# Optimization experiments

Measured on AMD Instinct MI355X. Metric: run time of the kernel, lower is better.

The kernel has to match this reference:

```python
import jax, jax.numpy as jnp
import numpy as np

B, S, D, H = 4, 2048, 1024, 16
DH = D // H
LN_EPS = 1e-5


def setup_inputs() -> dict:
    key = jax.random.key(0)
    ks = jax.random.split(key, 8)
    q = jax.random.normal(ks[0], (B, S, D), dtype=jnp.float32)
    k = jax.random.normal(ks[1], (B, S, D), dtype=jnp.float32)
    v = jax.random.normal(ks[2], (B, S, D), dtype=jnp.float32)
    masks = jax.random.randint(ks[3], (B, S, S), 0, 2, dtype=jnp.int32)
    proj_Q = jax.random.normal(ks[4], (D,), dtype=jnp.float32)
    proj_K = jax.random.normal(ks[5], (D,), dtype=jnp.float32)
    proj_V = jax.random.normal(ks[6], (D,), dtype=jnp.float32)
    gamma = jnp.ones((D,), dtype=jnp.float32)
    beta = jnp.zeros((D,), dtype=jnp.float32)
    return {"q": q, "k": k, "v": v, "masks": masks,
            "proj_Q": proj_Q, "proj_K": proj_K, "proj_V": proj_V,
            "gamma": gamma, "beta": beta}


def _split_heads(x):
    # x: [B,S,D] -> permute(0,2,1) -> [B,D,S] -> view(B*H, DH, S) -> permute -> [B*H, S, DH]
    xt = jnp.transpose(x, (0, 2, 1))              # [B,D,S]
    xt = xt.reshape(B * H, DH, S)                 # [B*H,DH,S] (batch-major head split)
    return jnp.transpose(xt, (0, 2, 1))           # [B*H,S,DH]


def reference(q, k, v, masks, proj_Q, proj_K, proj_V, gamma, beta):
    # Source bug preserved: projections all applied to `x` == q; k, v are ignored.
    x = q
    Qh = _split_heads(x * proj_Q)                 # [B*H,S,DH]
    Kh = _split_heads(x * proj_K)
    Vh = _split_heads(x * proj_V)

    # masks cat'd along dim 0 num_head times (head-major tiling, as in source)
    m = jnp.tile(masks, (H, 1, 1)).astype(bool)   # [H*B,S,S]

    scores = jnp.einsum('nqd,nkd->nqk', Qh, Kh) / jnp.sqrt(jnp.float32(D))
    scores = jnp.where(m, jnp.float32(-1e-10), scores)  # source uses -1e-10, not -inf
    attn = jax.nn.softmax(scores, axis=2)
    ctx = jnp.einsum('nqk,nkd->nqd', attn, Vh)    # [B*H,S,DH]

    # merge heads back: [B*H,S,DH] -> [B*H,DH,S] -> [B,D,S] -> [B,S,D]
    ctx = jnp.transpose(ctx, (0, 2, 1)).reshape(B, D, S)
    ctx = jnp.transpose(ctx, (0, 2, 1))

    out = ctx + q                                  # dropout(p=0) is identity
    mu = jnp.mean(out, axis=-1, keepdims=True)
    var = jnp.var(out, axis=-1, keepdims=True)
    out = (out - mu) * jax.lax.rsqrt(var + LN_EPS) * gamma + beta
    return out
```

## Files before the change

### kernel.cpp

```cpp
#include <hip/hip_runtime.h>
#include <math.h>

#define Bn 4
#define Sn 2048
#define Dn 1024
#define Hn 16
#define DHn 64
#define QT 128
#define KT 64
#define STR 72

typedef __attribute__((ext_vector_type(8))) short short8;
typedef __attribute__((ext_vector_type(4))) float f32x4;

__device__ __forceinline__ ushort f2bf(float f) {
    union { float f; unsigned u; } x; x.f = f;
    unsigned r = x.u + 0x7fffu + ((x.u >> 16) & 1u);
    return (ushort)(r >> 16);
}

__device__ __forceinline__ unsigned pack_bf2(float lo, float hi) {
    unsigned r;
    asm("v_cvt_pk_bf16_f32 %0, %1, %2" : "=v"(r) : "v"(lo), "v"(hi));
    return r;
}

__device__ __forceinline__ float fexp2(float x) { return __builtin_amdgcn_exp2f(x); }

__device__ __forceinline__ float mask_sel(unsigned nib, int r, float s) {
    int sx; unsigned tb;
    asm("v_bfe_i32 %0, %1, %2, 1" : "=v"(sx) : "v"(nib), "i"(r));
    asm("v_bfi_b32 %0, %1, 0, %2" : "=v"(tb) : "v"(sx), "v"(__float_as_uint(s)));
    return __uint_as_float(tb);
}

__global__ __launch_bounds__(256)
void prep_fused(const float* __restrict__ xin, const float* __restrict__ pK,
                const float* __restrict__ pV, const int* __restrict__ masks,
                ushort* __restrict__ Kw, ushort* __restrict__ Vw,
                unsigned long long* __restrict__ mpack)
{
    __shared__ ushort LK[64 * STR];
    __shared__ ushort LV[64 * STR];
    const int t = threadIdx.x;

    if (blockIdx.x >= 2048) {
        const int l = t & 63;
        const int wid_g = ((blockIdx.x - 2048) * 256 + t) >> 6;
        #pragma unroll 4
        for (int i = 0; i < 16; ++i) {
            int word = wid_g * 16 + i;
            int row  = word >> 5, wd = word & 31;
            int m = masks[(size_t)row * 2048 + wd * 64 + l];
            unsigned long long bits = __ballot(m != 0);
            if (l == 0) mpack[word] = bits;
        }
        return;
    }

    const int kt = blockIdx.x & 31, n = blockIdx.x >> 5, b = n >> 4, h = n & 15;
    const int sl = t >> 2, dq = (t & 3) * 16;

    const float* xp  = xin + ((size_t)b * Sn + kt * 64 + sl) * Dn + h * DHn + dq;
    const float* pkp = pK + h * DHn + dq;
    const float* pvp = pV + h * DHn + dq;

    float xv[16], pk[16], pv[16];
    #pragma unroll
    for (int j = 0; j < 4; ++j) {
        float4 a  = ((const float4*)xp)[j];
        float4 kk = ((const float4*)pkp)[j];
        float4 vv = ((const float4*)pvp)[j];
        xv[4*j+0] = a.x;  xv[4*j+1] = a.y;  xv[4*j+2] = a.z;  xv[4*j+3] = a.w;
        pk[4*j+0] = kk.x; pk[4*j+1] = kk.y; pk[4*j+2] = kk.z; pk[4*j+3] = kk.w;
        pv[4*j+0] = vv.x; pv[4*j+1] = vv.y; pv[4*j+2] = vv.z; pv[4*j+3] = vv.w;
    }
    unsigned kw[8], vw[8];
    #pragma unroll
    for (int j = 0; j < 8; ++j) {
        kw[j] = pack_bf2(xv[2*j] * pk[2*j], xv[2*j+1] * pk[2*j+1]);
        vw[j] = pack_bf2(xv[2*j] * pv[2*j], xv[2*j+1] * pv[2*j+1]);
    }
    *(uint4*)&LK[sl * STR + dq]     = make_uint4(kw[0], kw[1], kw[2], kw[3]);
    *(uint4*)&LK[sl * STR + dq + 8] = make_uint4(kw[4], kw[5], kw[6], kw[7]);
    *(uint4*)&LV[sl * STR + dq]     = make_uint4(vw[0], vw[1], vw[2], vw[3]);
    *(uint4*)&LV[sl * STR + dq + 8] = make_uint4(vw[4], vw[5], vw[6], vw[7]);
    __syncthreads();

    ushort* kout = Kw + ((size_t)n * 32 + kt) * 4096;
    ushort* vout = Vw + ((size_t)n * 32 + kt) * 4096;
    #pragma unroll
    for (int i = 0; i < 2; ++i) {
        int c  = t * 2 + i;
        int f  = c >> 6, lc = c & 63;
        int key = (f >> 1) * 16 + (lc & 15);
        int dh0 = (f & 1) * 32 + (lc >> 4) * 8;
        *(uint4*)(kout + c * 8) = *(const uint4*)&LK[key * STR + dh0];
        int dg = f & 3, hh = f >> 2;
        int dhv = dg * 16 + (lc & 15);
        ushort tmp[8];
        #pragma unroll
        for (int e = 0; e < 8; ++e) {
            int p  = hh * 32 + (lc >> 4) * 8 + e;
            int ss = (p & 32) | ((p & 4) << 2) | ((p & 24) >> 1) | (p & 3);
            tmp[e] = LV[ss * STR + dhv];
        }
        unsigned o0 = (unsigned)tmp[0] | ((unsigned)tmp[1] << 16);
        unsigned o1 = (unsigned)tmp[2] | ((unsigned)tmp[3] << 16);
        unsigned o2 = (unsigned)tmp[4] | ((unsigned)tmp[5] << 16);
        unsigned o3 = (unsigned)tmp[6] | ((unsigned)tmp[7] << 16);
        *(uint4*)(vout + c * 8) = make_uint4(o0, o1, o2, o3);
    }
}

__global__ __launch_bounds__(256, 3)
void attn_fast3(const float* __restrict__ xin, const unsigned long long* __restrict__ mpack,
                const float* __restrict__ pQ, const ushort* __restrict__ Kw,
                const ushort* __restrict__ Vw, float* __restrict__ out)
{
    __shared__ __attribute__((aligned(16))) ushort S[16384];

    const int id   = blockIdx.x;
    const int xcd  = id & 7, pos = id >> 3;
    const int n    = (pos >> 4) * 8 + xcd;
    const int q0   = (pos & 15) * 128;
    const int b    = n >> 4;
    const int h    = n & 15;
    const int mb   = n & 3;

    const int t  = threadIdx.x;
    const int w  = t >> 6;
    const int l  = t & 63;
    const int G  = l >> 4;
    const int li = l & 15;
    const int G4 = G * 4;
    const int G4p16 = G4 + 16;

    const float C2 = 0.0450842200277800f;
    const float* xb = xin + (size_t)b * Sn * Dn + h * DHn;
    const float pq_s = pQ[h * DHn + l] * C2;
    #pragma unroll
    for (int i = 0; i < 8; ++i) {
        #pragma unroll
        for (int j = 0; j < 4; ++j) {
            int qr = i * 4 + j;
            float v = xb[(size_t)(q0 + w * 32 + qr) * Dn + l];
            S[(w * 32 + qr) * STR + l] = f2bf(v * pq_s);
        }
    }
    short8 qf[2][2];
    #pragma unroll
    for (int qs = 0; qs < 2; ++qs)
        #pragma unroll
        for (int kk = 0; kk < 2; ++kk)
            qf[qs][kk] = *(const short8*)&S[(w*32 + qs*16 + li) * STR + kk*32 + G*8];
    __syncthreads();

    const f32x4 Z4 = {0.f, 0.f, 0.f, 0.f};
    const short8 VONES = {(short)0x3F80, (short)0x3F80, (short)0x3F80, (short)0x3F80,
                          (short)0x3F80, (short)0x3F80, (short)0x3F80, (short)0x3F80};

    f32x4 acc_o[2][4];
    f32x4 acc_l[2];
    #pragma unroll
    for (int qs = 0; qs < 2; ++qs) {
        #pragma unroll
        for (int dg = 0; dg < 4; ++dg) acc_o[qs][dg] = (f32x4){0.f, 0.f, 0.f, 0.f};
        acc_l[qs] = (f32x4){0.f, 0.f, 0.f, 0.f};
    }

    const ushort* kwf = Kw + (size_t)n * 131072 + (w * 2) * 512 + (size_t)l * 8;
    const ushort* vwf = Vw + (size_t)n * 131072 + (w * 2) * 512 + (size_t)l * 8;
    const int fo0 = (w * 2) * 512 + l * 8;
    const int fo1 = (w * 2 + 1) * 512 + l * 8;

    const int row0 = q0 + w * 32 + li;
    const unsigned long long* mrow0 = mpack + (size_t)(mb * 2048 + row0) * 32;
    const unsigned long long* mrow1 = mpack + (size_t)(mb * 2048 + row0 + 16) * 32;

    unsigned long long mA0, mA1, mB0, mB1;

    {
        short8 a = *(const short8*)kwf;
        short8 c = *(const short8*)(kwf + 512);
        short8 d = *(const short8*)vwf;
        short8 e = *(const short8*)(vwf + 512);
        mA0 = mrow0[0]; mA1 = mrow1[0];
        *(short8*)&S[fo0] = a;
        *(short8*)&S[fo1] = c;
        *(short8*)&S[8192 + fo0] = d;
        *(short8*)&S[8192 + fo1] = e;
    }

#define BODY(CUR, NXT, MC0, MC1, MN0, MN1, KTv, PF)                                   \
    {                                                                                  \
        __syncthreads();                     \
               \
        f32x4 s_[2][4];                                                                \
        __builtin_amdgcn_s_setprio(1);                                                 \
        _Pragma("unroll")                                                              \
        for (int kg = 0; kg < 4; ++kg) {                                               \
            short8 kf0 = *(const short8*)&S[(CUR)*4096 + (kg*2+0)*512 + l*8];          \
            short8 kf1 = *(const short8*)&S[(CUR)*4096 + (kg*2+1)*512 + l*8];          \
            s_[0][kg] = __builtin_amdgcn_mfma_f32_16x16x32_bf16(kf0, qf[0][0], Z4, 0, 0, 0); \
            s_[1][kg] = __builtin_amdgcn_mfma_f32_16x16x32_bf16(kf0, qf[1][0], Z4, 0, 0, 0); \
            s_[0][kg] = __builtin_amdgcn_mfma_f32_16x16x32_bf16(kf1, qf[0][1], s_[0][kg], 0, 0, 0); \
            s_[1][kg] = __builtin_amdgcn_mfma_f32_16x16x32_bf16(kf1, qf[1][1], s_[1][kg], 0, 0, 0); \
        }                                                                              \
        __builtin_amdgcn_s_setprio(0);                                                 \
                        \
        short8 kst0, kst1, vst0, vst1;                                                 \
        if (PF) {                                                                      \
            const ushort* kp = kwf + (size_t)((KTv)+1) * 4096;                         \
            const ushort* vp = vwf + (size_t)((KTv)+1) * 4096;                         \
            kst0 = *(const short8*)kp;  kst1 = *(const short8*)(kp + 512);             \
            vst0 = *(const short8*)vp;  vst1 = *(const short8*)(vp + 512);             \
            MN0 = mrow0[(KTv)+1];       MN1 = mrow1[(KTv)+1];                          \
        }                                                                              \
                       \
        short8 pf[2][2];                                                               \
        _Pragma("unroll")                                                              \
        for (int qs = 0; qs < 2; ++qs) {                                               \
            unsigned mlo = (unsigned)(qs ? (MC1) : (MC0));                             \
            unsigned mhi = (unsigned)((qs ? (MC1) : (MC0)) >> 32);                     \
            float ev[16];                                                              \
            _Pragma("unroll")                                                          \
            for (int kg = 0; kg < 4; ++kg) {                                           \
                unsigned dwh = (kg < 2) ? mlo : mhi;                                   \
                unsigned nib;                                                          \
                asm("v_bfe_u32 %0, %1, %2, 4" : "=v"(nib)                              \
                    : "v"(dwh), "v"((kg & 1) ? G4p16 : G4));                           \
                _Pragma("unroll")                                                      \
                for (int r = 0; r < 4; ++r)                                            \
                    ev[kg*4 + r] = fexp2(mask_sel(nib, r, s_[qs][kg][r]));             \
            }                                                                          \
            _Pragma("unroll")                                                          \
            for (int hh = 0; hh < 2; ++hh) {                                           \
                union { unsigned u[4]; short8 v; } pu;                                 \
                pu.u[0] = pack_bf2(ev[hh*8+0], ev[hh*8+1]);                            \
                pu.u[1] = pack_bf2(ev[hh*8+2], ev[hh*8+3]);                            \
                pu.u[2] = pack_bf2(ev[hh*8+4], ev[hh*8+5]);                            \
                pu.u[3] = pack_bf2(ev[hh*8+6], ev[hh*8+7]);                            \
                pf[qs][hh] = pu.v;                                                     \
            }                                                                          \
        }                                                                              \
                                                \
        __builtin_amdgcn_s_setprio(1);                                                 \
        _Pragma("unroll")                                                              \
        for (int hh = 0; hh < 2; ++hh) {                                               \
            short8 vf0 = *(const short8*)&S[8192 + (CUR)*4096 + (hh*4+0)*512 + l*8];   \
            short8 vf1 = *(const short8*)&S[8192 + (CUR)*4096 + (hh*4+1)*512 + l*8];   \
            short8 vf2 = *(const short8*)&S[8192 + (CUR)*4096 + (hh*4+2)*512 + l*8];   \
            short8 vf3 = *(const short8*)&S[8192 + (CUR)*4096 + (hh*4+3)*512 + l*8];   \
            _Pragma("unroll")                                                          \
            for (int qs = 0; qs < 2; ++qs) {                                           \
                acc_o[qs][0] = __builtin_amdgcn_mfma_f32_16x16x32_bf16(pf[qs][hh], vf0, acc_o[qs][0], 0, 0, 0); \
                acc_o[qs][1] = __builtin_amdgcn_mfma_f32_16x16x32_bf16(pf[qs][hh], vf1, acc_o[qs][1], 0, 0, 0); \
                acc_o[qs][2] = __builtin_amdgcn_mfma_f32_16x16x32_bf16(pf[qs][hh], vf2, acc_o[qs][2], 0, 0, 0); \
                acc_o[qs][3] = __builtin_amdgcn_mfma_f32_16x16x32_bf16(pf[qs][hh], vf3, acc_o[qs][3], 0, 0, 0); \
                acc_l[qs]    = __builtin_amdgcn_mfma_f32_16x16x32_bf16(pf[qs][hh], VONES, acc_l[qs], 0, 0, 0); \
            }                                                                          \
        }                                                                              \
        __builtin_amdgcn_s_setprio(0);                                                 \
                                     \
        if (PF) {                                                                      \
            *(short8*)&S[(NXT)*4096 + fo0] = kst0;                                     \
            *(short8*)&S[(NXT)*4096 + fo1] = kst1;                                     \
            *(short8*)&S[8192 + (NXT)*4096 + fo0] = vst0;                              \
            *(short8*)&S[8192 + (NXT)*4096 + fo1] = vst1;                              \
        }                                                                              \
    }

    for (int kt = 0; kt < 32; kt += 2) {
        BODY(0, 1, mA0, mA1, mB0, mB1, kt, true)
        BODY(1, 0, mB0, mB1, mA0, mA1, kt + 1, (kt + 1 < 31))
    }
#undef BODY

    #pragma unroll
    for (int qs = 0; qs < 2; ++qs) {
        #pragma unroll
        for (int r = 0; r < 4; ++r) {
            float inv = 1.f / acc_l[qs][r];
            int qg = q0 + w*32 + qs*16 + G4 + r;
            float* ob = out + ((size_t)b * Sn + qg) * Dn + h * DHn;
            #pragma unroll
            for (int dg = 0; dg < 4; ++dg)
                ob[dg*16 + li] = acc_o[qs][dg][r] * inv;
        }
    }
}

__global__ __launch_bounds__(256)
void prep_kv(const float* __restrict__ xin, const float* __restrict__ pK,
             const float* __restrict__ pV, ushort* __restrict__ Kbf,
             ushort* __restrict__ Vtw)
{
    __shared__ ushort Ls[64 * STR];
    const int n = blockIdx.y, b = n >> 4, h = n & 15;
    const int s0 = blockIdx.x * 64;
    const int t = threadIdx.x;
    const int sl = t >> 2, dq = (t & 3) * 16;

    const float* xp = xin + (size_t)b * Sn * Dn + (size_t)(s0 + sl) * Dn + h * DHn + dq;
    const float* pkp = pK + h * DHn + dq;
    const float* pvp = pV + h * DHn + dq;

    float xv[16], pk[16], pv[16];
    #pragma unroll
    for (int j = 0; j < 4; ++j) {
        float4 a = ((const float4*)xp)[j];
        float4 kk = ((const float4*)pkp)[j];
        float4 vv = ((const float4*)pvp)[j];
        xv[4*j+0] = a.x;  xv[4*j+1] = a.y;  xv[4*j+2] = a.z;  xv[4*j+3] = a.w;
        pk[4*j+0] = kk.x; pk[4*j+1] = kk.y; pk[4*j+2] = kk.z; pk[4*j+3] = kk.w;
        pv[4*j+0] = vv.x; pv[4*j+1] = vv.y; pv[4*j+2] = vv.z; pv[4*j+3] = vv.w;
    }
    unsigned kw[8], vw[8];
    #pragma unroll
    for (int j = 0; j < 8; ++j) {
        kw[j] = pack_bf2(xv[2*j] * pk[2*j], xv[2*j+1] * pk[2*j+1]);
        vw[j] = pack_bf2(xv[2*j] * pv[2*j], xv[2*j+1] * pv[2*j+1]);
    }
    ushort* kdst = Kbf + ((size_t)n * Sn + s0 + sl) * DHn + dq;
    *(uint4*)kdst       = make_uint4(kw[0], kw[1], kw[2], kw[3]);
    *(uint4*)(kdst + 8) = make_uint4(kw[4], kw[5], kw[6], kw[7]);

    *(uint4*)&Ls[sl * STR + dq]     = make_uint4(vw[0], vw[1], vw[2], vw[3]);
    *(uint4*)&Ls[sl * STR + dq + 8] = make_uint4(vw[4], vw[5], vw[6], vw[7]);
    __syncthreads();

    const int dh = t >> 2, p4 = t & 3;
    ushort ov[16];
    #pragma unroll
    for (int j = 0; j < 16; ++j) {
        int p  = p4 * 16 + j;
        int ss = (p & 32) | ((p & 4) << 2) | ((p & 24) >> 1) | (p & 3);
        ov[j] = Ls[ss * STR + dh];
    }
    unsigned ow[8];
    #pragma unroll
    for (int j = 0; j < 8; ++j) ow[j] = (unsigned)ov[2*j] | ((unsigned)ov[2*j+1] << 16);
    ushort* vdst = Vtw + ((size_t)n * DHn + dh) * Sn + s0 + p4 * 16;
    *(uint4*)vdst       = make_uint4(ow[0], ow[1], ow[2], ow[3]);
    *(uint4*)(vdst + 8) = make_uint4(ow[4], ow[5], ow[6], ow[7]);
}

__global__ __launch_bounds__(256, 4)
void attn_fast2(const float* __restrict__ xin, const int* __restrict__ masks,
                const float* __restrict__ pQ, const ushort* __restrict__ Kbf,
                const ushort* __restrict__ Vtw, float* __restrict__ out)
{
    __shared__ ushort Ks[KT * STR];
    __shared__ ushort Vts[DHn * STR];

    const int n  = blockIdx.y;
    const int b  = n >> 4;
    const int h  = n & 15;
    const int mb = n & 3;
    const int q0 = blockIdx.x * QT;

    const int t  = threadIdx.x;
    const int w  = t >> 6;
    const int l  = t & 63;
    const int G  = l >> 4;
    const int li = l & 15;

    const float C2 = 0.0450842200277800f;
    const float* xb = xin + (size_t)b * Sn * Dn + h * DHn;
    const float pq_s = pQ[h * DHn + l] * C2;
    ushort* qstage = ((w < 2) ? Ks : Vts) + (w & 1) * (32 * STR);
    #pragma unroll
    for (int i = 0; i < 8; ++i) {
        #pragma unroll
        for (int j = 0; j < 4; ++j) {
            int qr = i * 4 + j;
            float v = xb[(size_t)(q0 + w * 32 + qr) * Dn + l];
            qstage[qr * STR + l] = f2bf(v * pq_s);
        }
    }
    short8 qf[2][2];
    #pragma unroll
    for (int qs = 0; qs < 2; ++qs)
        #pragma unroll
        for (int kk = 0; kk < 2; ++kk)
            qf[qs][kk] = *(const short8*)&qstage[(qs*16 + li) * STR + kk*32 + G*8];

    f32x4 acc_o[2][4];
    float lsum[2];
    #pragma unroll
    for (int qs = 0; qs < 2; ++qs) {
        #pragma unroll
        for (int dg = 0; dg < 4; ++dg) acc_o[qs][dg] = (f32x4){0.f, 0.f, 0.f, 0.f};
        lsum[qs] = 0.f;
    }

    const int* mq = masks + (size_t)mb * Sn * Sn + (size_t)(q0 + w*32 + li) * Sn;

    const int srow = w * 16 + (l >> 2);
    const int part = (l & 3) * 16;
    const ushort* ksrc = Kbf + (size_t)n * Sn * DHn + (size_t)srow * DHn + part;
    const ushort* vsrc = Vtw + (size_t)n * DHn * Sn + (size_t)srow * Sn + part;
    ushort* kdst = &Ks[srow * STR + part];
    ushort* vdst = &Vts[srow * STR + part];

    for (int kt = 0; kt < Sn / KT; ++kt) {
        __syncthreads();
        const ushort* kp = ksrc + (size_t)kt * KT * DHn;
        const ushort* vp = vsrc + kt * KT;
        short8 k0 = *(const short8*)kp, k1 = *(const short8*)(kp + 8);
        short8 v0 = *(const short8*)vp, v1 = *(const short8*)(vp + 8);
        *(short8*)kdst       = k0;
        *(short8*)(kdst + 8) = k1;
        *(short8*)vdst       = v0;
        *(short8*)(vdst + 8) = v1;
        __syncthreads();

        f32x4 s[2][4];
        #pragma unroll
        for (int qs = 0; qs < 2; ++qs)
            #pragma unroll
            for (int kg = 0; kg < 4; ++kg) s[qs][kg] = (f32x4){0.f, 0.f, 0.f, 0.f};
        __builtin_amdgcn_s_setprio(1);
        #pragma unroll
        for (int kg = 0; kg < 4; ++kg) {
            #pragma unroll
            for (int kk = 0; kk < 2; ++kk) {
                short8 kf = *(const short8*)&Ks[(kg*16 + li) * STR + kk*32 + G*8];
                s[0][kg] = __builtin_amdgcn_mfma_f32_16x16x32_bf16(kf, qf[0][kk], s[0][kg], 0, 0, 0);
                s[1][kg] = __builtin_amdgcn_mfma_f32_16x16x32_bf16(kf, qf[1][kk], s[1][kg], 0, 0, 0);
            }
        }
        __builtin_amdgcn_s_setprio(0);

        short8 pf[2][2];
        #pragma unroll
        for (int qs = 0; qs < 2; ++qs) {
            int4 mv[4];
            #pragma unroll
            for (int kg = 0; kg < 4; ++kg)
                mv[kg] = *(const int4*)(mq + (size_t)qs*16*Sn + kt*KT + kg*16 + G*4);
            float ev[16];
            #pragma unroll
            for (int kg = 0; kg < 4; ++kg) {
                int ma[4] = {mv[kg].x, mv[kg].y, mv[kg].z, mv[kg].w};
                #pragma unroll
                for (int r = 0; r < 4; ++r) {
                    float tt = ma[r] ? 0.f : s[qs][kg][r];
                    ev[kg*4 + r] = fexp2(tt);
                }
            }
            lsum[qs] += (((ev[0]+ev[1])+(ev[2]+ev[3])) + ((ev[4]+ev[5])+(ev[6]+ev[7])))
                      + (((ev[8]+ev[9])+(ev[10]+ev[11])) + ((ev[12]+ev[13])+(ev[14]+ev[15])));
            #pragma unroll
            for (int hh = 0; hh < 2; ++hh) {
                union { unsigned u[4]; short8 v; } pu;
                pu.u[0] = pack_bf2(ev[hh*8+0], ev[hh*8+1]);
                pu.u[1] = pack_bf2(ev[hh*8+2], ev[hh*8+3]);
                pu.u[2] = pack_bf2(ev[hh*8+4], ev[hh*8+5]);
                pu.u[3] = pack_bf2(ev[hh*8+6], ev[hh*8+7]);
                pf[qs][hh] = pu.v;
            }
        }

        #pragma unroll
        for (int hh = 0; hh < 2; ++hh) {
            short8 vf[4];
            #pragma unroll
            for (int dg = 0; dg < 4; ++dg)
                vf[dg] = *(const short8*)&Vts[(dg*16 + li) * STR + hh*32 + G*8];
            __builtin_amdgcn_s_setprio(1);
            #pragma unroll
            for (int qs = 0; qs < 2; ++qs)
                #pragma unroll
                for (int dg = 0; dg < 4; ++dg)
                    acc_o[qs][dg] = __builtin_amdgcn_mfma_f32_16x16x32_bf16(pf[qs][hh], vf[dg], acc_o[qs][dg], 0, 0, 0);
            __builtin_amdgcn_s_setprio(0);
        }
    }

    #pragma unroll
    for (int qs = 0; qs < 2; ++qs) {
        float v = lsum[qs];
        v += __shfl_xor(v, 16, 64);
        v += __shfl_xor(v, 32, 64);
        lsum[qs] = v;
    }

    #pragma unroll
    for (int qs = 0; qs < 2; ++qs) {
        #pragma unroll
        for (int r = 0; r < 4; ++r) {
            float lv = __shfl(lsum[qs], (l & 48) | (G * 4 + r), 64);
            float inv = 1.f / lv;
            int qg = q0 + w*32 + qs*16 + G*4 + r;
            float* ob = out + ((size_t)b * Sn + qg) * Dn + h * DHn;
            #pragma unroll
            for (int dg = 0; dg < 4; ++dg)
                ob[dg*16 + li] = acc_o[qs][dg][r] * inv;
        }
    }
}

__global__ __launch_bounds__(256)
void ln_kernel(const float* __restrict__ qin, const float* __restrict__ gamma,
               const float* __restrict__ beta, float* __restrict__ out)
{
    const int row = blockIdx.x;
    const int t   = threadIdx.x;
    const size_t base = (size_t)row * Dn + t * 4;

    float4 c = *(const float4*)(out + base);
    float4 r = *(const float4*)(qin + base);
    float4 v = make_float4(c.x + r.x, c.y + r.y, c.z + r.z, c.w + r.w);

    float sum = v.x + v.y + v.z + v.w;
    float sq  = v.x * v.x + v.y * v.y + v.z * v.z + v.w * v.w;
    #pragma unroll
    for (int off = 32; off >= 1; off >>= 1) {
        sum += __shfl_xor(sum, off, 64);
        sq  += __shfl_xor(sq,  off, 64);
    }
    __shared__ float as_[4], aq_[4];
    const int wid = t >> 6, ln = t & 63;
    if (ln == 0) { as_[wid] = sum; aq_[wid] = sq; }
    __syncthreads();
    sum = as_[0] + as_[1] + as_[2] + as_[3];
    sq  = aq_[0] + aq_[1] + aq_[2] + aq_[3];

    const float mean = sum * (1.f / Dn);
    const float var  = sq * (1.f / Dn) - mean * mean;
    const float rstd = rsqrtf(var + 1e-5f);

    float4 ga = *(const float4*)(gamma + t * 4);
    float4 be = *(const float4*)(beta + t * 4);
    float4 o;
    o.x = (v.x - mean) * rstd * ga.x + be.x;
    o.y = (v.y - mean) * rstd * ga.y + be.y;
    o.z = (v.z - mean) * rstd * ga.z + be.z;
    o.w = (v.w - mean) * rstd * ga.w + be.w;
    *(float4*)(out + base) = o;
}

extern "C" void kernel_launch(void* const* d_in, const int* in_sizes, int n_in,
                              void* d_out, int out_size, void* d_ws, size_t ws_size,
                              hipStream_t stream) {
    const float* q     = (const float*)d_in[0];
    const int*   masks = (const int*)d_in[3];
    const float* pQ    = (const float*)d_in[4];
    const float* pK    = (const float*)d_in[5];
    const float* pV    = (const float*)d_in[6];
    const float* gamma = (const float*)d_in[7];
    const float* beta  = (const float*)d_in[8];
    float* out = (float*)d_out;
    (void)in_sizes; (void)n_in; (void)out_size;

    const size_t elems = (size_t)Bn * Hn * Sn * DHn;
    const size_t kvbytes = elems * 2 * sizeof(ushort);
    const size_t need3 = kvbytes + (size_t)4 * Sn * 32 * 8;

    if (ws_size >= need3) {
        ushort* Kw = (ushort*)d_ws;
        ushort* Vw = Kw + elems;
        unsigned long long* mpack = (unsigned long long*)((char*)d_ws + kvbytes);
        prep_fused<<<6144, 256, 0, stream>>>(q, pK, pV, masks, Kw, Vw, mpack);
        attn_fast3<<<1024, 256, 0, stream>>>(q, mpack, pQ, Kw, Vw, out);
    } else if (ws_size >= kvbytes) {
        ushort* Kbf = (ushort*)d_ws;
        ushort* Vtw = Kbf + elems;
        prep_kv<<<dim3(Sn / 64, Bn * Hn), 256, 0, stream>>>(q, pK, pV, Kbf, Vtw);
        attn_fast2<<<dim3(Sn / QT, Bn * Hn), 256, 0, stream>>>(q, masks, pQ, Kbf, Vtw, out);
    }
    ln_kernel<<<Bn * Sn, 256, 0, stream>>>(q, gamma, beta, out);
}
```

Before: 137.9 us.

## Load K/V fragments directly from global memory instead of staging through LDS

New measurement: 146.8 us. 1.06x slower.

```diff
diff --git a/kernel.cpp b/kernel.cpp
--- a/kernel.cpp
+++ b/kernel.cpp
@@ -114,11 +114,11 @@
 }
 
 __global__ __launch_bounds__(256, 3)
-void attn_fast3(const float* __restrict__ xin, const unsigned long long* __restrict__ mpack,
+void attn_fast4(const float* __restrict__ xin, const unsigned long long* __restrict__ mpack,
                 const float* __restrict__ pQ, const ushort* __restrict__ Kw,
                 const ushort* __restrict__ Vw, float* __restrict__ out)
 {
-    __shared__ __attribute__((aligned(16))) ushort S[16384];
+    __shared__ __attribute__((aligned(16))) ushort S[QT * STR];
 
     const int id   = blockIdx.x;
     const int xcd  = id & 7, pos = id >> 3;
@@ -154,7 +154,6 @@
         #pragma unroll
         for (int kk = 0; kk < 2; ++kk)
             qf[qs][kk] = *(const short8*)&S[(w*32 + qs*16 + li) * STR + kk*32 + G*8];
-    __syncthreads();
 
     const f32x4 Z4 = {0.f, 0.f, 0.f, 0.f};
     const short8 VONES = {(short)0x3F80, (short)0x3F80, (short)0x3F80, (short)0x3F80,
@@ -169,113 +168,78 @@
         acc_l[qs] = (f32x4){0.f, 0.f, 0.f, 0.f};
     }
 
-    const ushort* kwf = Kw + (size_t)n * 131072 + (w * 2) * 512 + (size_t)l * 8;
-    const ushort* vwf = Vw + (size_t)n * 131072 + (w * 2) * 512 + (size_t)l * 8;
-    const int fo0 = (w * 2) * 512 + l * 8;
-    const int fo1 = (w * 2 + 1) * 512 + l * 8;
+    const ushort* kwb = Kw + (size_t)n * 131072 + (size_t)l * 8;
+    const ushort* vwb = Vw + (size_t)n * 131072 + (size_t)l * 8;
 
     const int row0 = q0 + w * 32 + li;
     const unsigned long long* mrow0 = mpack + (size_t)(mb * 2048 + row0) * 32;
     const unsigned long long* mrow1 = mpack + (size_t)(mb * 2048 + row0 + 16) * 32;
 
-    unsigned long long mA0, mA1, mB0, mB1;
-
-    {
-        short8 a = *(const short8*)kwf;
-        short8 c = *(const short8*)(kwf + 512);
-        short8 d = *(const short8*)vwf;
-        short8 e = *(const short8*)(vwf + 512);
-        mA0 = mrow0[0]; mA1 = mrow1[0];
-        *(short8*)&S[fo0] = a;
-        *(short8*)&S[fo1] = c;
-        *(short8*)&S[8192 + fo0] = d;
-        *(short8*)&S[8192 + fo1] = e;
-    }
-
-#define BODY(CUR, NXT, MC0, MC1, MN0, MN1, KTv, PF)                                   \
-    {                                                                                  \
-        __syncthreads();                     \
-               \
-        f32x4 s_[2][4];                                                                \
-        __builtin_amdgcn_s_setprio(1);                                                 \
-        _Pragma("unroll")                                                              \
-        for (int kg = 0; kg < 4; ++kg) {                                               \
-            short8 kf0 = *(const short8*)&S[(CUR)*4096 + (kg*2+0)*512 + l*8];          \
-            short8 kf1 = *(const short8*)&S[(CUR)*4096 + (kg*2+1)*512 + l*8];          \
-            s_[0][kg] = __builtin_amdgcn_mfma_f32_16x16x32_bf16(kf0, qf[0][0], Z4, 0, 0, 0); \
-            s_[1][kg] = __builtin_amdgcn_mfma_f32_16x16x32_bf16(kf0, qf[1][0], Z4, 0, 0, 0); \
-            s_[0][kg] = __builtin_amdgcn_mfma_f32_16x16x32_bf16(kf1, qf[0][1], s_[0][kg], 0, 0, 0); \
-            s_[1][kg] = __builtin_amdgcn_mfma_f32_16x16x32_bf16(kf1, qf[1][1], s_[1][kg], 0, 0, 0); \
-        }                                                                              \
-        __builtin_amdgcn_s_setprio(0);                                                 \
-                        \
-        short8 kst0, kst1, vst0, vst1;                                                 \
-        if (PF) {                                                                      \
-            const ushort* kp = kwf + (size_t)((KTv)+1) * 4096;                         \
-            const ushort* vp = vwf + (size_t)((KTv)+1) * 4096;                         \
-            kst0 = *(const short8*)kp;  kst1 = *(const short8*)(kp + 512);             \
-            vst0 = *(const short8*)vp;  vst1 = *(const short8*)(vp + 512);             \
-            MN0 = mrow0[(KTv)+1];       MN1 = mrow1[(KTv)+1];                          \
-        }                                                                              \
-                       \
-        short8 pf[2][2];                                                               \
-        _Pragma("unroll")                                                              \
-        for (int qs = 0; qs < 2; ++qs) {                                               \
-            unsigned mlo = (unsigned)(qs ? (MC1) : (MC0));                             \
-            unsigned mhi = (unsigned)((qs ? (MC1) : (MC0)) >> 32);                     \
-            float ev[16];                                                              \
-            _Pragma("unroll")                                                          \
-            for (int kg = 0; kg < 4; ++kg) {                                           \
-                unsigned dwh = (kg < 2) ? mlo : mhi;                                   \
-                unsigned nib;                                                          \
-                asm("v_bfe_u32 %0, %1, %2, 4" : "=v"(nib)                              \
-                    : "v"(dwh), "v"((kg & 1) ? G4p16 : G4));                           \
-                _Pragma("unroll")                                                      \
-                for (int r = 0; r < 4; ++r)                                            \
-                    ev[kg*4 + r] = fexp2(mask_sel(nib, r, s_[qs][kg][r]));             \
-            }                                                                          \
-            _Pragma("unroll")                                                          \
-            for (int hh = 0; hh < 2; ++hh) {                                           \
-                union { unsigned u[4]; short8 v; } pu;                                 \
-                pu.u[0] = pack_bf2(ev[hh*8+0], ev[hh*8+1]);                            \
-                pu.u[1] = pack_bf2(ev[hh*8+2], ev[hh*8+3]);                            \
-                pu.u[2] = pack_bf2(ev[hh*8+4], ev[hh*8+5]);                            \
-                pu.u[3] = pack_bf2(ev[hh*8+6], ev[hh*8+7]);                            \
-                pf[qs][hh] = pu.v;                                                     \
-            }                                                                          \
-        }                                                                              \
-                                                \
-        __builtin_amdgcn_s_setprio(1);                                                 \
-        _Pragma("unroll")                                                              \
-        for (int hh = 0; hh < 2; ++hh) {                                               \
-            short8 vf0 = *(const short8*)&S[8192 + (CUR)*4096 + (hh*4+0)*512 + l*8];   \
-            short8 vf1 = *(const short8*)&S[8192 + (CUR)*4096 + (hh*4+1)*512 + l*8];   \
-            short8 vf2 = *(const short8*)&S[8192 + (CUR)*4096 + (hh*4+2)*512 + l*8];   \
-            short8 vf3 = *(const short8*)&S[8192 + (CUR)*4096 + (hh*4+3)*512 + l*8];   \
-            _Pragma("unroll")                                                          \
-            for (int qs = 0; qs < 2; ++qs) {                                           \
-                acc_o[qs][0] = __builtin_amdgcn_mfma_f32_16x16x32_bf16(pf[qs][hh], vf0, acc_o[qs][0], 0, 0, 0); \
-                acc_o[qs][1] = __builtin_amdgcn_mfma_f32_16x16x32_bf16(pf[qs][hh], vf1, acc_o[qs][1], 0, 0, 0); \
-                acc_o[qs][2] = __builtin_amdgcn_mfma_f32_16x16x32_bf16(pf[qs][hh], vf2, acc_o[qs][2], 0, 0, 0); \
-                acc_o[qs][3] = __builtin_amdgcn_mfma_f32_16x16x32_bf16(pf[qs][hh], vf3, acc_o[qs][3], 0, 0, 0); \
-                acc_l[qs]    = __builtin_amdgcn_mfma_f32_16x16x32_bf16(pf[qs][hh], VONES, acc_l[qs], 0, 0, 0); \
-            }                                                                          \
-        }                                                                              \
-        __builtin_amdgcn_s_setprio(0);                                                 \
-                                     \
-        if (PF) {                                                                      \
-            *(short8*)&S[(NXT)*4096 + fo0] = kst0;                                     \
-            *(short8*)&S[(NXT)*4096 + fo1] = kst1;                                     \
-            *(short8*)&S[8192 + (NXT)*4096 + fo0] = vst0;                              \
-            *(short8*)&S[8192 + (NXT)*4096 + fo1] = vst1;                              \
-        }                                                                              \
-    }
-
-    for (int kt = 0; kt < 32; kt += 2) {
-        BODY(0, 1, mA0, mA1, mB0, mB1, kt, true)
-        BODY(1, 0, mB0, mB1, mA0, mA1, kt + 1, (kt + 1 < 31))
-    }
-#undef BODY
+    #pragma unroll 2
+    for (int kt = 0; kt < 32; ++kt) {
+        const ushort* kp = kwb + kt * 4096;
+        const ushort* vp = vwb + kt * 4096;
+        unsigned long long mc0 = mrow0[kt];
+        unsigned long long mc1 = mrow1[kt];
+
+        f32x4 s_[2][4];
+        __builtin_amdgcn_s_setprio(1);
+        #pragma unroll
+        for (int kg = 0; kg < 4; ++kg) {
+            short8 kf0 = *(const short8*)(kp + (kg*2+0)*512);
+            short8 kf1 = *(const short8*)(kp + (kg*2+1)*512);
+            s_[0][kg] = __builtin_amdgcn_mfma_f32_16x16x32_bf16(kf0, qf[0][0], Z4, 0, 0, 0);
+            s_[1][kg] = __builtin_amdgcn_mfma_f32_16x16x32_bf16(kf0, qf[1][0], Z4, 0, 0, 0);
+            s_[0][kg] = __builtin_amdgcn_mfma_f32_16x16x32_bf16(kf1, qf[0][1], s_[0][kg], 0, 0, 0);
+            s_[1][kg] = __builtin_amdgcn_mfma_f32_16x16x32_bf16(kf1, qf[1][1], s_[1][kg], 0, 0, 0);
+        }
+        __builtin_amdgcn_s_setprio(0);
+
+        short8 pf[2][2];
+        #pragma unroll
+        for (int qs = 0; qs < 2; ++qs) {
+            unsigned mlo = (unsigned)(qs ? mc1 : mc0);
+            unsigned mhi = (unsigned)((qs ? mc1 : mc0) >> 32);
+            float ev[16];
+            #pragma unroll
+            for (int kg = 0; kg < 4; ++kg) {
+                unsigned dwh = (kg < 2) ? mlo : mhi;
+                unsigned nib;
+                asm("v_bfe_u32 %0, %1, %2, 4" : "=v"(nib)
+                    : "v"(dwh), "v"((kg & 1) ? G4p16 : G4));
+                #pragma unroll
+                for (int r = 0; r < 4; ++r)
+                    ev[kg*4 + r] = fexp2(mask_sel(nib, r, s_[qs][kg][r]));
+            }
+            #pragma unroll
+            for (int hh = 0; hh < 2; ++hh) {
+                union { unsigned u[4]; short8 v; } pu;
+                pu.u[0] = pack_bf2(ev[hh*8+0], ev[hh*8+1]);
+                pu.u[1] = pack_bf2(ev[hh*8+2], ev[hh*8+3]);
+                pu.u[2] = pack_bf2(ev[hh*8+4], ev[hh*8+5]);
+                pu.u[3] = pack_bf2(ev[hh*8+6], ev[hh*8+7]);
+                pf[qs][hh] = pu.v;
+            }
+        }
+
+        __builtin_amdgcn_s_setprio(1);
+        #pragma unroll
+        for (int hh = 0; hh < 2; ++hh) {
+            short8 vf0 = *(const short8*)(vp + (hh*4+0)*512);
+            short8 vf1 = *(const short8*)(vp + (hh*4+1)*512);
+            short8 vf2 = *(const short8*)(vp + (hh*4+2)*512);
+            short8 vf3 = *(const short8*)(vp + (hh*4+3)*512);
+            #pragma unroll
+            for (int qs = 0; qs < 2; ++qs) {
+                acc_o[qs][0] = __builtin_amdgcn_mfma_f32_16x16x32_bf16(pf[qs][hh], vf0, acc_o[qs][0], 0, 0, 0);
+                acc_o[qs][1] = __builtin_amdgcn_mfma_f32_16x16x32_bf16(pf[qs][hh], vf1, acc_o[qs][1], 0, 0, 0);
+                acc_o[qs][2] = __builtin_amdgcn_mfma_f32_16x16x32_bf16(pf[qs][hh], vf2, acc_o[qs][2], 0, 0, 0);
+                acc_o[qs][3] = __builtin_amdgcn_mfma_f32_16x16x32_bf16(pf[qs][hh], vf3, acc_o[qs][3], 0, 0, 0);
+                acc_l[qs]    = __builtin_amdgcn_mfma_f32_16x16x32_bf16(pf[qs][hh], VONES, acc_l[qs], 0, 0, 0);
+            }
+        }
+        __builtin_amdgcn_s_setprio(0);
+    }
 
     #pragma unroll
     for (int qs = 0; qs < 2; ++qs) {
@@ -564,7 +528,7 @@
         ushort* Vw = Kw + elems;
         unsigned long long* mpack = (unsigned long long*)((char*)d_ws + kvbytes);
         prep_fused<<<6144, 256, 0, stream>>>(q, pK, pV, masks, Kw, Vw, mpack);
-        attn_fast3<<<1024, 256, 0, stream>>>(q, mpack, pQ, Kw, Vw, out);
+        attn_fast4<<<1024, 256, 0, stream>>>(q, mpack, pQ, Kw, Vw, out);
     } else if (ws_size >= kvbytes) {
         ushort* Kbf = (ushort*)d_ws;
         ushort* Vtw = Kbf + elems;
```

## Load K/V fragments directly from global into registers, drop LDS staging

Applied to the files above, without the earlier changes.

New measurement: 146.6 us. 6.3% more time.

```diff
diff --git a/kernel.cpp b/kernel.cpp
--- a/kernel.cpp
+++ b/kernel.cpp
@@ -113,12 +113,12 @@
     }
 }
 
-__global__ __launch_bounds__(256, 3)
-void attn_fast3(const float* __restrict__ xin, const unsigned long long* __restrict__ mpack,
+__global__ __launch_bounds__(256, 2)
+void attn_fast5(const float* __restrict__ xin, const unsigned long long* __restrict__ mpack,
                 const float* __restrict__ pQ, const ushort* __restrict__ Kw,
                 const ushort* __restrict__ Vw, float* __restrict__ out)
 {
-    __shared__ __attribute__((aligned(16))) ushort S[16384];
+    __shared__ __attribute__((aligned(16))) ushort S[QT * STR];
 
     const int id   = blockIdx.x;
     const int xcd  = id & 7, pos = id >> 3;
@@ -154,7 +154,6 @@
         #pragma unroll
         for (int kk = 0; kk < 2; ++kk)
             qf[qs][kk] = *(const short8*)&S[(w*32 + qs*16 + li) * STR + kk*32 + G*8];
-    __syncthreads();
 
     const f32x4 Z4 = {0.f, 0.f, 0.f, 0.f};
     const short8 VONES = {(short)0x3F80, (short)0x3F80, (short)0x3F80, (short)0x3F80,
@@ -169,54 +168,46 @@
         acc_l[qs] = (f32x4){0.f, 0.f, 0.f, 0.f};
     }
 
-    const ushort* kwf = Kw + (size_t)n * 131072 + (w * 2) * 512 + (size_t)l * 8;
-    const ushort* vwf = Vw + (size_t)n * 131072 + (w * 2) * 512 + (size_t)l * 8;
-    const int fo0 = (w * 2) * 512 + l * 8;
-    const int fo1 = (w * 2 + 1) * 512 + l * 8;
+    const ushort* kwb = Kw + (size_t)n * 131072 + (size_t)l * 8;
+    const ushort* vwb = Vw + (size_t)n * 131072 + (size_t)l * 8;
 
     const int row0 = q0 + w * 32 + li;
     const unsigned long long* mrow0 = mpack + (size_t)(mb * 2048 + row0) * 32;
     const unsigned long long* mrow1 = mpack + (size_t)(mb * 2048 + row0 + 16) * 32;
 
+    short8 kA[8], vA[8], kB[8], vB[8];
     unsigned long long mA0, mA1, mB0, mB1;
-
-    {
-        short8 a = *(const short8*)kwf;
-        short8 c = *(const short8*)(kwf + 512);
-        short8 d = *(const short8*)vwf;
-        short8 e = *(const short8*)(vwf + 512);
-        mA0 = mrow0[0]; mA1 = mrow1[0];
-        *(short8*)&S[fo0] = a;
-        *(short8*)&S[fo1] = c;
-        *(short8*)&S[8192 + fo0] = d;
-        *(short8*)&S[8192 + fo1] = e;
-    }
-
-#define BODY(CUR, NXT, MC0, MC1, MN0, MN1, KTv, PF)                                   \
+    #pragma unroll
+    for (int f = 0; f < 8; ++f) {
+        kA[f] = *(const short8*)(kwb + f * 512);
+        vA[f] = *(const short8*)(vwb + f * 512);
+    }
+    mA0 = mrow0[0]; mA1 = mrow1[0];
+
+#define BODY(KC, VC, KN, VN, MC0, MC1, MN0, MN1, KTv, PF)                              \
     {                                                                                  \
-        __syncthreads();                     \
+                  \
+        if (PF) {                                                                      \
+            const ushort* kp = kwb + (size_t)((KTv)+1) * 4096;                         \
+            const ushort* vp = vwb + (size_t)((KTv)+1) * 4096;                         \
+            _Pragma("unroll")                                                          \
+            for (int f = 0; f < 8; ++f) {                                              \
+                KN[f] = *(const short8*)(kp + f * 512);                                \
+                VN[f] = *(const short8*)(vp + f * 512);                                \
+            }                                                                          \
+            MN0 = mrow0[(KTv)+1];  MN1 = mrow1[(KTv)+1];                               \
+        }                                                                              \
                \
         f32x4 s_[2][4];                                                                \
         __builtin_amdgcn_s_setprio(1);                                                 \
         _Pragma("unroll")                                                              \
         for (int kg = 0; kg < 4; ++kg) {                                               \
-            short8 kf0 = *(const short8*)&S[(CUR)*4096 + (kg*2+0)*512 + l*8];          \
-            short8 kf1 = *(const short8*)&S[(CUR)*4096 + (kg*2+1)*512 + l*8];          \
-            s_[0][kg] = __builtin_amdgcn_mfma_f32_16x16x32_bf16(kf0, qf[0][0], Z4, 0, 0, 0); \
-            s_[1][kg] = __builtin_amdgcn_mfma_f32_16x16x32_bf16(kf0, qf[1][0], Z4, 0, 0, 0); \
-            s_[0][kg] = __builtin_amdgcn_mfma_f32_16x16x32_bf16(kf1, qf[0][1], s_[0][kg], 0, 0, 0); \
-            s_[1][kg] = __builtin_amdgcn_mfma_f32_16x16x32_bf16(kf1, qf[1][1], s_[1][kg], 0, 0, 0); \
+            s_[0][kg] = __builtin_amdgcn_mfma_f32_16x16x32_bf16(KC[kg*2+0], qf[0][0], Z4, 0, 0, 0); \
+            s_[1][kg] = __builtin_amdgcn_mfma_f32_16x16x32_bf16(KC[kg*2+0], qf[1][0], Z4, 0, 0, 0); \
+            s_[0][kg] = __builtin_amdgcn_mfma_f32_16x16x32_bf16(KC[kg*2+1], qf[0][1], s_[0][kg], 0, 0, 0); \
+            s_[1][kg] = __builtin_amdgcn_mfma_f32_16x16x32_bf16(KC[kg*2+1], qf[1][1], s_[1][kg], 0, 0, 0); \
         }                                                                              \
         __builtin_amdgcn_s_setprio(0);                                                 \
-                        \
-        short8 kst0, kst1, vst0, vst1;                                                 \
-        if (PF) {                                                                      \
-            const ushort* kp = kwf + (size_t)((KTv)+1) * 4096;                         \
-            const ushort* vp = vwf + (size_t)((KTv)+1) * 4096;                         \
-            kst0 = *(const short8*)kp;  kst1 = *(const short8*)(kp + 512);             \
-            vst0 = *(const short8*)vp;  vst1 = *(const short8*)(vp + 512);             \
-            MN0 = mrow0[(KTv)+1];       MN1 = mrow1[(KTv)+1];                          \
-        }                                                                              \
                        \
         short8 pf[2][2];                                                               \
         _Pragma("unroll")                                                              \
@@ -248,32 +239,21 @@
         __builtin_amdgcn_s_setprio(1);                                                 \
         _Pragma("unroll")                                                              \
         for (int hh = 0; hh < 2; ++hh) {                                               \
-            short8 vf0 = *(const short8*)&S[8192 + (CUR)*4096 + (hh*4+0)*512 + l*8];   \
-            short8 vf1 = *(const short8*)&S[8192 + (CUR)*4096 + (hh*4+1)*512 + l*8];   \
-            short8 vf2 = *(const short8*)&S[8192 + (CUR)*4096 + (hh*4+2)*512 + l*8];   \
-            short8 vf3 = *(const short8*)&S[8192 + (CUR)*4096 + (hh*4+3)*512 + l*8];   \
             _Pragma("unroll")                                                          \
             for (int qs = 0; qs < 2; ++qs) {                                           \
-                acc_o[qs][0] = __builtin_amdgcn_mfma_f32_16x16x32_bf16(pf[qs][hh], vf0, acc_o[qs][0], 0, 0, 0); \
-                acc_o[qs][1] = __builtin_amdgcn_mfma_f32_16x16x32_bf16(pf[qs][hh], vf1, acc_o[qs][1], 0, 0, 0); \
-                acc_o[qs][2] = __builtin_amdgcn_mfma_f32_16x16x32_bf16(pf[qs][hh], vf2, acc_o[qs][2], 0, 0, 0); \
-                acc_o[qs][3] = __builtin_amdgcn_mfma_f32_16x16x32_bf16(pf[qs][hh], vf3, acc_o[qs][3], 0, 0, 0); \
+                acc_o[qs][0] = __builtin_amdgcn_mfma_f32_16x16x32_bf16(pf[qs][hh], VC[hh*4+0], acc_o[qs][0], 0, 0, 0); \
+                acc_o[qs][1] = __builtin_amdgcn_mfma_f32_16x16x32_bf16(pf[qs][hh], VC[hh*4+1], acc_o[qs][1], 0, 0, 0); \
+                acc_o[qs][2] = __builtin_amdgcn_mfma_f32_16x16x32_bf16(pf[qs][hh], VC[hh*4+2], acc_o[qs][2], 0, 0, 0); \
+                acc_o[qs][3] = __builtin_amdgcn_mfma_f32_16x16x32_bf16(pf[qs][hh], VC[hh*4+3], acc_o[qs][3], 0, 0, 0); \
                 acc_l[qs]    = __builtin_amdgcn_mfma_f32_16x16x32_bf16(pf[qs][hh], VONES, acc_l[qs], 0, 0, 0); \
             }                                                                          \
         }                                                                              \
         __builtin_amdgcn_s_setprio(0);                                                 \
-                                     \
-        if (PF) {                                                                      \
-            *(short8*)&S[(NXT)*4096 + fo0] = kst0;                                     \
-            *(short8*)&S[(NXT)*4096 + fo1] = kst1;                                     \
-            *(short8*)&S[8192 + (NXT)*4096 + fo0] = vst0;                              \
-            *(short8*)&S[8192 + (NXT)*4096 + fo1] = vst1;                              \
-        }                                                                              \
     }
 
     for (int kt = 0; kt < 32; kt += 2) {
-        BODY(0, 1, mA0, mA1, mB0, mB1, kt, true)
-        BODY(1, 0, mB0, mB1, mA0, mA1, kt + 1, (kt + 1 < 31))
+        BODY(kA, vA, kB, vB, mA0, mA1, mB0, mB1, kt, true)
+        BODY(kB, vB, kA, vA, mB0, mB1, mA0, mA1, kt + 1, (kt + 1 < 31))
     }
 #undef BODY
 
@@ -564,7 +544,7 @@
         ushort* Vw = Kw + elems;
         unsigned long long* mpack = (unsigned long long*)((char*)d_ws + kvbytes);
         prep_fused<<<6144, 256, 0, stream>>>(q, pK, pV, masks, Kw, Vw, mpack);
-        attn_fast3<<<1024, 256, 0, stream>>>(q, mpack, pQ, Kw, Vw, out);
+        attn_fast5<<<1024, 256, 0, stream>>>(q, mpack, pQ, Kw, Vw, out);
     } else if (ws_size >= kvbytes) {
         ushort* Kbf = (ushort*)d_ws;
         ushort* Vtw = Kbf + elems;
```
